# Optimization experiments

Hardware: AMD Instinct MI355X
Metric: run time of the kernel (lower is better)

The kernel has to match this reference:

```python
import jax, jax.numpy as jnp
import numpy as np

N = 50000      # nodes
E = 400000     # edges per edge type
T = 4          # edge types: add/sub/mul/div
F_IN = 128     # in_channels
H = 2          # heads
C = 64         # hidden_channels (per head)
HC = H * C     # 128
MLP = C // 8   # hidden_channels // 8 = 8
NUM_CLASSES = 10


def _glorot(key, shape):
    fan_in, fan_out = shape[-2], shape[-1]
    s = jnp.sqrt(6.0 / (fan_in + fan_out))
    return jax.random.uniform(key, shape, jnp.float32, -s, s)


def setup_inputs() -> dict:
    key = jax.random.key(0)
    ks = jax.random.split(key, 12)
    x = jax.random.normal(ks[0], (N, F_IN), jnp.float32)
    edge_index = jax.random.randint(ks[1], (T, 2, E), 0, N, jnp.int32)
    # layer-1 GATv2 params, stacked over the 4 edge types
    Wl1 = _glorot(ks[2], (T, F_IN, HC))
    Wr1 = _glorot(ks[3], (T, F_IN, HC))
    att1 = _glorot(ks[4], (T, H, C))
    b1 = jnp.zeros((T, HC), jnp.float32)
    # layer-2 GATv2 params (input dim = hidden*heads)
    Wl2 = _glorot(ks[5], (T, HC, HC))
    Wr2 = _glorot(ks[6], (T, HC, HC))
    att2 = _glorot(ks[7], (T, H, C))
    b2 = jnp.zeros((T, HC), jnp.float32)
    # MLP head
    W_lin1 = _glorot(ks[8], (HC, MLP))
    b_lin1 = jnp.zeros((MLP,), jnp.float32)
    W_lin2 = _glorot(ks[9], (MLP, NUM_CLASSES))
    b_lin2 = jnp.zeros((NUM_CLASSES,), jnp.float32)
    return dict(x=x, edge_index=edge_index, Wl1=Wl1, Wr1=Wr1, att1=att1, b1=b1,
                Wl2=Wl2, Wr2=Wr2, att2=att2, b2=b2,
                W_lin1=W_lin1, b_lin1=b_lin1, W_lin2=W_lin2, b_lin2=b_lin2)


def gatv2_conv(x, src, dst, Wl, Wr, att, bias):
    """PyG GATv2Conv: add self-loops, per-edge LeakyReLU attention,
    softmax over incoming edges per destination, weighted scatter-add."""
    n = x.shape[0]
    xl = (x @ Wl).reshape(n, H, C)   # source transform
    xr = (x @ Wr).reshape(n, H, C)   # destination transform
    loop = jnp.arange(n, dtype=src.dtype)
    s = jnp.concatenate([src, loop])
    d = jnp.concatenate([dst, loop])
    e = jax.nn.leaky_relu(xl[s] + xr[d], 0.2)          # [E+n, H, C]
    score = jnp.einsum('ehc,hc->eh', e, att)           # [E+n, H]
    smax = jax.ops.segment_max(score, d, num_segments=n)  # [N, H]
    p = jnp.exp(score - smax[d])                       # stable softmax numerators
    denom = jax.ops.segment_sum(p, d, num_segments=n)  # [N, H]
    msg = jax.ops.segment_sum(p[:, :, None] * xl[s], d, num_segments=n)  # [N, H, C]
    out = msg / denom[:, :, None]
    return out.reshape(n, HC) + bias


def hetero_layer(x, edge_index, Wl, Wr, att, b):
    # HeteroConv with aggr='sum' over the 4 edge types (single node type)
    out = gatv2_conv(x, edge_index[0, 0], edge_index[0, 1], Wl[0], Wr[0], att[0], b[0])
    for t in range(1, T):
        out = out + gatv2_conv(x, edge_index[t, 0], edge_index[t, 1], Wl[t], Wr[t], att[t], b[t])
    return out


def reference(x, edge_index, Wl1, Wr1, att1, b1, Wl2, Wr2, att2, b2,
              W_lin1, b_lin1, W_lin2, b_lin2):
    h = jax.nn.relu(hetero_layer(x, edge_index, Wl1, Wr1, att1, b1))
    h = jax.nn.relu(hetero_layer(h, edge_index, Wl2, Wr2, att2, b2))
    h = jax.nn.relu(h @ W_lin1 + b_lin1)
    # dropout p=0.5 is identity at eval time
    return h @ W_lin2 + b_lin2
```

## Files before the change

kernel.cpp:

```cpp
#include <hip/hip_runtime.h>
#include <hip/hip_bf16.h>
#include <math.h>

#define NN 50000
#define EE 400000
#define TT 4
#define FD 128
#define RPS 50004
#define NBKT 196
#define BCAP 4096
#define LOG2E 1.44269504f

typedef __attribute__((ext_vector_type(8))) short bf16x8;
typedef __attribute__((ext_vector_type(4))) float f32x4;

__device__ inline float bf2f(unsigned short u) {
  union { unsigned int i; float f; } x; x.i = ((unsigned int)u) << 16; return x.f;
}
__device__ inline unsigned short f2bf(float f) {
  __hip_bfloat16 h = __float2bfloat16(f);
  unsigned short u; __builtin_memcpy(&u, &h, 2); return u;
}
__device__ inline float blo(unsigned int u) {
  union { unsigned int i; float f; } x; x.i = u << 16; return x.f;
}
__device__ inline float bhi(unsigned int u) {
  union { unsigned int i; float f; } x; x.i = u & 0xFFFF0000u; return x.f;
}
__device__ inline float fexp2(float x) { return __builtin_amdgcn_exp2f(x); }
__device__ inline float sgn04(float a) {
  union { float f; unsigned int i; } x; x.f = a;
  x.i = (x.i & 0x80000000u) | 0x3ECCCCCDu;
  return x.f;
}
__device__ inline float qsum16(float v) {
  v += __builtin_bit_cast(float, __builtin_amdgcn_update_dpp(
         0, __builtin_bit_cast(int, v), 0xB1, 0xF, 0xF, true));
  v += __builtin_bit_cast(float, __builtin_amdgcn_update_dpp(
         0, __builtin_bit_cast(int, v), 0x4E, 0xF, 0xF, true));
  v += __builtin_bit_cast(float, __builtin_amdgcn_update_dpp(
         0, __builtin_bit_cast(int, v), 0x141, 0xF, 0xF, true));
  v += __builtin_bit_cast(float, __builtin_amdgcn_update_dpp(
         0, __builtin_bit_cast(int, v), 0x140, 0xF, 0xF, true));
  return v;
}

__global__ void k_cvtW(const float* __restrict__ Wl1, const float* __restrict__ Wr1,
                       const float* __restrict__ Wl2, const float* __restrict__ Wr2,
                       unsigned short* __restrict__ Bpack) {
  const int idx = blockIdx.x * 256 + threadIdx.x;
  const int R = idx >> 14;
  const int kc = idx & 16383;
  const int lr = R & 1, t = (R >> 1) & 3, layer = R >> 3;
  const float* W = layer ? (lr ? Wr2 : Wl2) : (lr ? Wr1 : Wl1);
  const float v = W[t * 16384 + kc];
  const int k = kc >> 7, c = kc & 127;
  const int nt = c >> 4, ks = k >> 5, g = (k >> 3) & 3, j = k & 7;
  const int lane = g * 16 + (c & 15);
  Bpack[(size_t)R * 16384 + ((nt * 4 + ks) * 64 + lane) * 8 + j] = f2bf(v);
}

__global__ void k_cvtA(const float* __restrict__ src, unsigned short* __restrict__ ahi,
                       unsigned short* __restrict__ alo) {
  const int idx = blockIdx.x * 256 + threadIdx.x;
  float4 v = ((const float4*)src)[idx];
  const unsigned short h0 = f2bf(v.x), h1 = f2bf(v.y), h2 = f2bf(v.z), h3 = f2bf(v.w);
  const unsigned short l0 = f2bf(v.x - bf2f(h0)), l1 = f2bf(v.y - bf2f(h1));
  const unsigned short l2 = f2bf(v.z - bf2f(h2)), l3 = f2bf(v.w - bf2f(h3));
  uint2 hv, lv;
  hv.x = (unsigned)h0 | ((unsigned)h1 << 16); hv.y = (unsigned)h2 | ((unsigned)h3 << 16);
  lv.x = (unsigned)l0 | ((unsigned)l1 << 16); lv.y = (unsigned)l2 | ((unsigned)l3 << 16);
  ((uint2*)ahi)[idx] = hv;
  ((uint2*)alo)[idx] = lv;
}

__global__ __launch_bounds__(128) void k_gemm4(
    const unsigned short* __restrict__ Ahi, const unsigned short* __restrict__ Alo,
    const unsigned short* __restrict__ Bbase,
    unsigned short* __restrict__ xl4, unsigned short* __restrict__ xr4) {
  const int t = blockIdx.y;
  const unsigned short* Bpt = Bbase + (size_t)t * 2 * 16384;
  unsigned short* xl = xl4 + (size_t)t * NN * FD;
  unsigned short* xr = xr4 + (size_t)t * NN * FD;
  const int tid = threadIdx.x;
  const int lane = tid & 63;
  const int w = tid >> 6;
  const int rh = lane & 15, g = lane >> 4;
  const int m0 = blockIdx.x * 64 + w * 32;
  f32x4 acc[2][16];
  #pragma unroll
  for (int a = 0; a < 2; ++a)
    #pragma unroll
    for (int b = 0; b < 16; ++b) acc[a][b] = (f32x4){0.f, 0.f, 0.f, 0.f};
  int r0 = m0 + rh;      if (r0 > NN - 1) r0 = NN - 1;
  int r1 = m0 + 16 + rh; if (r1 > NN - 1) r1 = NN - 1;
  #pragma unroll
  for (int ks = 0; ks < 4; ++ks) {
    const int ko = ks * 32 + g * 8;
    const bf16x8 ah0 = *(const bf16x8*)(Ahi + (size_t)r0 * FD + ko);
    const bf16x8 al0 = *(const bf16x8*)(Alo + (size_t)r0 * FD + ko);
    const bf16x8 ah1 = *(const bf16x8*)(Ahi + (size_t)r1 * FD + ko);
    const bf16x8 al1 = *(const bf16x8*)(Alo + (size_t)r1 * FD + ko);
    #pragma unroll
    for (int nt = 0; nt < 16; ++nt) {
      const bf16x8 b = *(const bf16x8*)(Bpt + (nt >> 3) * 16384 +
                                        (((nt & 7) * 4 + ks) * 64 + lane) * 8);
      acc[0][nt] = __builtin_amdgcn_mfma_f32_16x16x32_bf16(ah0, b, acc[0][nt], 0, 0, 0);
      acc[0][nt] = __builtin_amdgcn_mfma_f32_16x16x32_bf16(al0, b, acc[0][nt], 0, 0, 0);
      acc[1][nt] = __builtin_amdgcn_mfma_f32_16x16x32_bf16(ah1, b, acc[1][nt], 0, 0, 0);
      acc[1][nt] = __builtin_amdgcn_mfma_f32_16x16x32_bf16(al1, b, acc[1][nt], 0, 0, 0);
    }
  }
  #pragma unroll
  for (int mt = 0; mt < 2; ++mt)
    #pragma unroll
    for (int nt = 0; nt < 16; ++nt) {
      unsigned short* op = (nt < 8) ? xl : xr;
      const int cb = (nt & 7) * 16 + rh;
      #pragma unroll
      for (int r = 0; r < 4; ++r) {
        const int row = m0 + mt * 16 + g * 4 + r;
        if (row < NN) op[(size_t)row * FD + cb] = f2bf(acc[mt][nt][r]);
      }
    }
}

__global__ __launch_bounds__(256) void k_bucket(const int* __restrict__ ei,
                                                int* __restrict__ bcur,
                                                unsigned int* __restrict__ ebuf) {
  __shared__ int lcnt[NBKT], lbase[NBKT];
  const int t = blockIdx.y, tid = threadIdx.x;
  const int cbase = blockIdx.x * 4096;
  if (tid < NBKT) lcnt[tid] = 0;
  __syncthreads();
  const int* srcp = ei + (size_t)t * 2 * EE;
  const int* dstp = srcp + EE;
  unsigned int pk[16]; int rk[16];
  #pragma unroll
  for (int i = 0; i < 16; ++i) {
    const int e = cbase + i * 256 + tid;
    rk[i] = -1;
    if (e < EE) {
      const int s = srcp[e], dd = dstp[e];
      const int b = dd >> 8;
      pk[i] = ((unsigned)dd << 16) | (unsigned)s;
      rk[i] = (atomicAdd(&lcnt[b], 1) << 8) | b;
    }
  }
  __syncthreads();
  if (tid < NBKT && lcnt[tid] > 0) lbase[tid] = atomicAdd(&bcur[t * NBKT + tid], lcnt[tid]);
  __syncthreads();
  #pragma unroll
  for (int i = 0; i < 16; ++i) {
    if (rk[i] >= 0) {
      const int b = rk[i] & 255, r = rk[i] >> 8;
      ebuf[((size_t)t * NBKT + b) * BCAP + lbase[b] + r] = pk[i];
    }
  }
}

__global__ void k_bktscan(const int* __restrict__ bcur, int* __restrict__ bbase) {
  __shared__ int s[TT * NBKT];
  const int tid = threadIdx.x;
  int v0 = 0;
  if (tid < TT * NBKT) { v0 = bcur[tid]; s[tid] = v0; }
  __syncthreads();
  #pragma unroll
  for (int off = 1; off < NBKT; off <<= 1) {
    int a = 0;
    if (tid < TT * NBKT && (tid % NBKT) >= off) a = s[tid - off];
    __syncthreads();
    if (tid < TT * NBKT) s[tid] += a;
    __syncthreads();
  }
  if (tid < TT * NBKT) bbase[tid] = s[tid] - v0;
}

__global__ __launch_bounds__(256) void k_scatter3(const unsigned int* __restrict__ ebuf,
                                                  const int* __restrict__ bcur,
                                                  const int* __restrict__ bbase,
                                                  int* __restrict__ rowp,
                                                  int* __restrict__ col) {
  __shared__ int lc[256], sc[256];
  const int b = blockIdx.x, t = blockIdx.y, tid = threadIdx.x;
  const int d0 = b << 8;
  const int nd = (NN - d0 < 256) ? (NN - d0) : 256;
  const int cnt = bcur[t * NBKT + b];
  const int base = bbase[t * NBKT + b];
  const unsigned int* eb = ebuf + ((size_t)t * NBKT + b) * BCAP;
  lc[tid] = 0;
  __syncthreads();
  for (int j = tid; j < cnt; j += 256) {
    atomicAdd(&lc[(eb[j] >> 16) - d0], 1);
  }
  __syncthreads();
  const int v = lc[tid];
  sc[tid] = v;
  __syncthreads();
  #pragma unroll
  for (int off = 1; off < 256; off <<= 1) {
    const int a = (tid >= off) ? sc[tid - off] : 0;
    __syncthreads();
    sc[tid] += a;
    __syncthreads();
  }
  const int excl = base + sc[tid] - v;
  if (tid < nd) rowp[(size_t)t * RPS + d0 + tid] = excl;
  if (b == NBKT - 1 && tid == 0) rowp[(size_t)t * RPS + NN] = EE;
  lc[tid] = excl;
  __syncthreads();
  for (int j = tid; j < cnt; j += 256) {
    const unsigned int u = eb[j];
    const int pos = atomicAdd(&lc[(u >> 16) - d0], 1);
    col[(size_t)t * EE + pos] = (int)(u & 0xFFFF);
  }
}

__global__ __launch_bounds__(256) void k_agg5(
    const unsigned short* __restrict__ xl4, const unsigned short* __restrict__ xr4,
    const int* __restrict__ col, const int* __restrict__ rowp,
    const float* __restrict__ att, const float* __restrict__ bias,
    unsigned short* __restrict__ ahi, unsigned short* __restrict__ alo,
    float* __restrict__ hout, const int mode) {
  const int lane = threadIdx.x & 63;
  const int d = blockIdx.x * 4 + (threadIdx.x >> 6);
  const int head = (lane >> 4) & 1, sub = lane & 15, pbit = lane >> 5;
  const int laneoff = head * 128 + sub * 8;
  const int choff = head * 64 + sub * 4;
  float o0 = 0.f, o1 = 0.f, o2 = 0.f, o3 = 0.f;
  for (int t = 0; t < TT; ++t) {
    const char* xlt = (const char*)xl4 + ((size_t)t * NN) * 256 + laneoff;
    const char* xrt = (const char*)xr4 + ((size_t)t * NN) * 256 + laneoff;
    const int* colt = col + (size_t)t * EE;
    float4 av = *(const float4*)(att + t * FD + choff);
    av.x *= LOG2E; av.y *= LOG2E; av.z *= LOG2E; av.w *= LOG2E;
    const float sa0 = sgn04(av.x), sa1 = sgn04(av.y);
    const float sa2 = sgn04(av.z), sa3 = sgn04(av.w);
    const uint2 ur = *(const uint2*)(xrt + (size_t)d * 256);
    const float axr0 = av.x * blo(ur.x), axr1 = av.y * bhi(ur.x);
    const float axr2 = av.z * blo(ur.y), axr3 = av.w * bhi(ur.y);
    const uint2 us = *(const uint2*)(xlt + (size_t)d * 256);
    const float xs0 = blo(us.x), xs1 = bhi(us.x), xs2 = blo(us.y), xs3 = bhi(us.y);
    {
      const float q0 = fmaf(av.x, xs0, axr0), q1 = fmaf(av.y, xs1, axr1);
      const float q2 = fmaf(av.z, xs2, axr2), q3 = fmaf(av.w, xs3, axr3);
      float r = sa0 * fabsf(q0);
      r = fmaf(sa1, fabsf(q1), r); r = fmaf(sa2, fabsf(q2), r); r = fmaf(sa3, fabsf(q3), r);
      const float c = qsum16(fmaf(0.6f, (q0 + q1) + (q2 + q3), r));
      const bool isA = (pbit == 0);
      float m = isA ? c : -3.0e38f;
      float den = isA ? 1.f : 0.f;
      float a0 = isA ? xs0 : 0.f, a1 = isA ? xs1 : 0.f;
      float a2 = isA ? xs2 : 0.f, a3 = isA ? xs3 : 0.f;
      const int beg = rowp[(size_t)t * RPS + d];
      const int end = rowp[(size_t)t * RPS + d + 1];
      for (int eb = beg; eb < end; eb += 2) {
        const int e = eb + pbit;
        const bool act = (e < end);
        const int ec = act ? e : end - 1;
        const int s = colt[ec];
        const uint2 u = *(const uint2*)(xlt + (size_t)s * 256);
        const float x0 = blo(u.x), x1 = bhi(u.x), x2 = blo(u.y), x3 = bhi(u.y);
        const float q0 = fmaf(av.x, x0, axr0), q1 = fmaf(av.y, x1, axr1);
        const float q2 = fmaf(av.z, x2, axr2), q3 = fmaf(av.w, x3, axr3);
        float r = sa0 * fabsf(q0);
        r = fmaf(sa1, fabsf(q1), r); r = fmaf(sa2, fabsf(q2), r); r = fmaf(sa3, fabsf(q3), r);
        float c2 = qsum16(fmaf(0.6f, (q0 + q1) + (q2 + q3), r));
        const float p = act ? c2 : -INFINITY;
        const float nm = fmaxf(m, p);
        const float scl = fexp2(m - nm), w = fexp2(p - nm);
        den = fmaf(den, scl, w);
        a0 = fmaf(a0, scl, w * x0); a1 = fmaf(a1, scl, w * x1);
        a2 = fmaf(a2, scl, w * x2); a3 = fmaf(a3, scl, w * x3);
        m = nm;
      }
      const float mo = __shfl_xor(m, 32), deno = __shfl_xor(den, 32);
      const float b0 = __shfl_xor(a0, 32), b1 = __shfl_xor(a1, 32);
      const float b2 = __shfl_xor(a2, 32), b3 = __shfl_xor(a3, 32);
      const float nm = fmaxf(m, mo);
      const float sMe = fexp2(m - nm), sOt = fexp2(mo - nm);
      const float dm = fmaf(den, sMe, deno * sOt);
      const float rden = __builtin_amdgcn_rcpf(dm);
      o0 = fmaf(fmaf(a0, sMe, b0 * sOt), rden, o0);
      o1 = fmaf(fmaf(a1, sMe, b1 * sOt), rden, o1);
      o2 = fmaf(fmaf(a2, sMe, b2 * sOt), rden, o2);
      o3 = fmaf(fmaf(a3, sMe, b3 * sOt), rden, o3);
    }
  }
  #pragma unroll
  for (int t = 0; t < TT; ++t) {
    const float4 bv = *(const float4*)(bias + t * FD + choff);
    o0 += bv.x; o1 += bv.y; o2 += bv.z; o3 += bv.w;
  }
  if (pbit == 0) {
    if (mode == 0) {
      o0 = fmaxf(o0, 0.f); o1 = fmaxf(o1, 0.f);
      o2 = fmaxf(o2, 0.f); o3 = fmaxf(o3, 0.f);
      const unsigned short h0 = f2bf(o0), h1 = f2bf(o1);
      const unsigned short h2 = f2bf(o2), h3 = f2bf(o3);
      const unsigned short l0 = f2bf(o0 - bf2f(h0)), l1 = f2bf(o1 - bf2f(h1));
      const unsigned short l2 = f2bf(o2 - bf2f(h2)), l3 = f2bf(o3 - bf2f(h3));
      uint2 hv, lv;
      hv.x = (unsigned)h0 | ((unsigned)h1 << 16); hv.y = (unsigned)h2 | ((unsigned)h3 << 16);
      lv.x = (unsigned)l0 | ((unsigned)l1 << 16); lv.y = (unsigned)l2 | ((unsigned)l3 << 16);
      const size_t ui = (size_t)d * 64 + head * 32 + sub * 2;
      ((uint2*)((unsigned int*)ahi + ui))[0] = hv;
      ((uint2*)((unsigned int*)alo + ui))[0] = lv;
    } else {
      *(float4*)(hout + (size_t)d * FD + choff) = make_float4(o0, o1, o2, o3);
    }
  }
}

__global__ __launch_bounds__(256) void k_mlp(const float* __restrict__ h,
                                             const float* __restrict__ W1,
                                             const float* __restrict__ b1,
                                             const float* __restrict__ W2,
                                             const float* __restrict__ b2,
                                             float* __restrict__ out) {
  __shared__ float sW1[128 * 8];
  __shared__ float sW2[8 * 10];
  __shared__ float sb1[8], sb2[10];
  for (int i = threadIdx.x; i < 1024; i += 256) sW1[i] = W1[i];
  if (threadIdx.x < 80) sW2[threadIdx.x] = W2[threadIdx.x];
  if (threadIdx.x < 8)  sb1[threadIdx.x] = b1[threadIdx.x];
  if (threadIdx.x < 10) sb2[threadIdx.x] = b2[threadIdx.x];
  __syncthreads();
  const int n = blockIdx.x * 256 + threadIdx.x;
  if (n >= NN) return;
  const float* hn = h + (size_t)n * FD;
  float z[8];
  #pragma unroll
  for (int j = 0; j < 8; ++j) z[j] = sb1[j];
  for (int k = 0; k < FD; k += 4) {
    float4 hv = *(const float4*)(hn + k);
    hv.x = fmaxf(hv.x, 0.f); hv.y = fmaxf(hv.y, 0.f);
    hv.z = fmaxf(hv.z, 0.f); hv.w = fmaxf(hv.w, 0.f);
    #pragma unroll
    for (int j = 0; j < 8; ++j) {
      z[j] += hv.x * sW1[(k + 0) * 8 + j] + hv.y * sW1[(k + 1) * 8 + j]
            + hv.z * sW1[(k + 2) * 8 + j] + hv.w * sW1[(k + 3) * 8 + j];
    }
  }
  #pragma unroll
  for (int j = 0; j < 8; ++j) z[j] = fmaxf(z[j], 0.f);
  float o[10];
  #pragma unroll
  for (int c = 0; c < 10; ++c) o[c] = sb2[c];
  #pragma unroll
  for (int j = 0; j < 8; ++j)
    #pragma unroll
    for (int c = 0; c < 10; ++c) o[c] += z[j] * sW2[j * 10 + c];
  float* op = out + (size_t)n * 10;
  #pragma unroll
  for (int c = 0; c < 10; ++c) op[c] = o[c];
}

extern "C" void kernel_launch(void* const* d_in, const int* in_sizes, int n_in,
                              void* d_out, int out_size, void* d_ws, size_t ws_size,
                              hipStream_t stream) {
  const float* x    = (const float*)d_in[0];
  const int*   ei   = (const int*)d_in[1];
  const float* Wl1  = (const float*)d_in[2];
  const float* Wr1  = (const float*)d_in[3];
  const float* att1 = (const float*)d_in[4];
  const float* b1   = (const float*)d_in[5];
  const float* Wl2  = (const float*)d_in[6];
  const float* Wr2  = (const float*)d_in[7];
  const float* att2 = (const float*)d_in[8];
  const float* b2   = (const float*)d_in[9];
  const float* Wi1  = (const float*)d_in[10];
  const float* bi1  = (const float*)d_in[11];
  const float* Wi2  = (const float*)d_in[12];
  const float* bi2  = (const float*)d_in[13];
  float* out = (float*)d_out;

  char* ws = (char*)d_ws;
  size_t off = 0;
  auto alloc = [&](size_t bytes) {
    void* p = ws + off;
    off = (off + bytes + 255) & ~(size_t)255;
    return p;
  };
  unsigned short* xl4   = (unsigned short*)alloc((size_t)TT * NN * FD * 2);
  unsigned short* xr4   = (unsigned short*)alloc((size_t)TT * NN * FD * 2);
  unsigned short* Ahi   = (unsigned short*)alloc((size_t)NN * FD * 2);
  unsigned short* Alo   = (unsigned short*)alloc((size_t)NN * FD * 2);
  unsigned short* Bpack = (unsigned short*)alloc((size_t)2 * TT * 2 * 16384 * 2);
  int*            col   = (int*)alloc((size_t)TT * EE * 4);
  int*            rowp  = (int*)alloc((size_t)TT * RPS * 4);
  int*            bcur  = (int*)alloc((size_t)TT * NBKT * 4);
  int*            bbase = (int*)alloc((size_t)TT * NBKT * 4);
  unsigned int*   ebuf  = (unsigned int*)alloc((size_t)TT * NBKT * BCAP * 4);
  float* h2 = (float*)Ahi;

  hipMemsetAsync(bcur, 0, (size_t)TT * NBKT * 4, stream);
  k_cvtW<<<1024, 256, 0, stream>>>(Wl1, Wr1, Wl2, Wr2, Bpack);
  k_bucket<<<dim3(98, TT), 256, 0, stream>>>(ei, bcur, ebuf);
  k_bktscan<<<1, 1024, 0, stream>>>(bcur, bbase);
  k_scatter3<<<dim3(NBKT, TT), 256, 0, stream>>>(ebuf, bcur, bbase, rowp, col);

  k_cvtA<<<6250, 256, 0, stream>>>(x, Ahi, Alo);
  k_gemm4<<<dim3(782, TT), 128, 0, stream>>>(Ahi, Alo, Bpack, xl4, xr4);
  k_agg5<<<12500, 256, 0, stream>>>(xl4, xr4, col, rowp, att1, b1,
                                    Ahi, Alo, nullptr, 0);
  k_gemm4<<<dim3(782, TT), 128, 0, stream>>>(Ahi, Alo, Bpack + (size_t)TT * 2 * 16384,
                                             xl4, xr4);
  k_agg5<<<12500, 256, 0, stream>>>(xl4, xr4, col, rowp, att2, b2,
                                    nullptr, nullptr, h2, 1);
  k_mlp<<<(NN + 255) / 256, 256, 0, stream>>>(h2, Wi1, bi1, Wi2, bi2, out);
}
```

Measured before the change: 570.6 us.

## Fold self-loops into CSR and aggregate four edges per wave without running max

```diff
diff --git a/kernel.cpp b/kernel.cpp
--- a/kernel.cpp
+++ b/kernel.cpp
@@ -4,6 +4,7 @@
 
 #define NN 50000
 #define EE 400000
+#define EEN 450000
 #define TT 4
 #define FD 128
 #define RPS 50004
@@ -33,16 +34,18 @@
   x.i = (x.i & 0x80000000u) | 0x3ECCCCCDu;
   return x.f;
 }
-__device__ inline float qsum16(float v) {
+__device__ inline float qsum8(float v) {
   v += __builtin_bit_cast(float, __builtin_amdgcn_update_dpp(
          0, __builtin_bit_cast(int, v), 0xB1, 0xF, 0xF, true));
   v += __builtin_bit_cast(float, __builtin_amdgcn_update_dpp(
          0, __builtin_bit_cast(int, v), 0x4E, 0xF, 0xF, true));
   v += __builtin_bit_cast(float, __builtin_amdgcn_update_dpp(
          0, __builtin_bit_cast(int, v), 0x141, 0xF, 0xF, true));
-  v += __builtin_bit_cast(float, __builtin_amdgcn_update_dpp(
-         0, __builtin_bit_cast(int, v), 0x140, 0xF, 0xF, true));
   return v;
+}
+__device__ inline void unpack8(const uint4 u, float* x) {
+  x[0] = blo(u.x); x[1] = bhi(u.x); x[2] = blo(u.y); x[3] = bhi(u.y);
+  x[4] = blo(u.z); x[5] = bhi(u.z); x[6] = blo(u.w); x[7] = bhi(u.w);
 }
 
 __global__ void k_cvtW(const float* __restrict__ Wl1, const float* __restrict__ Wr1,
@@ -140,8 +143,10 @@
   for (int i = 0; i < 16; ++i) {
     const int e = cbase + i * 256 + tid;
     rk[i] = -1;
-    if (e < EE) {
-      const int s = srcp[e], dd = dstp[e];
+    if (e < EEN) {
+      int s, dd;
+      if (e < EE) { s = srcp[e]; dd = dstp[e]; }
+      else        { s = dd = e - EE; }
       const int b = dd >> 8;
       pk[i] = ((unsigned)dd << 16) | (unsigned)s;
       rk[i] = (atomicAdd(&lcnt[b], 1) << 8) | b;
@@ -206,17 +211,17 @@
   }
   const int excl = base + sc[tid] - v;
   if (tid < nd) rowp[(size_t)t * RPS + d0 + tid] = excl;
-  if (b == NBKT - 1 && tid == 0) rowp[(size_t)t * RPS + NN] = EE;
+  if (b == NBKT - 1 && tid == 0) rowp[(size_t)t * RPS + NN] = EEN;
   lc[tid] = excl;
   __syncthreads();
   for (int j = tid; j < cnt; j += 256) {
     const unsigned int u = eb[j];
     const int pos = atomicAdd(&lc[(u >> 16) - d0], 1);
-    col[(size_t)t * EE + pos] = (int)(u & 0xFFFF);
-  }
-}
-
-__global__ __launch_bounds__(256) void k_agg5(
+    col[(size_t)t * EEN + pos] = (int)(u & 0xFFFF);
+  }
+}
+
+__global__ __launch_bounds__(256) void k_agg6(
     const unsigned short* __restrict__ xl4, const unsigned short* __restrict__ xr4,
     const int* __restrict__ col, const int* __restrict__ rowp,
     const float* __restrict__ att, const float* __restrict__ bias,
@@ -224,90 +229,93 @@
     float* __restrict__ hout, const int mode) {
   const int lane = threadIdx.x & 63;
   const int d = blockIdx.x * 4 + (threadIdx.x >> 6);
-  const int head = (lane >> 4) & 1, sub = lane & 15, pbit = lane >> 5;
-  const int laneoff = head * 128 + sub * 8;
-  const int choff = head * 64 + sub * 4;
-  float o0 = 0.f, o1 = 0.f, o2 = 0.f, o3 = 0.f;
+  const int g = lane >> 3;
+  const int slot = g >> 1, head = g & 1, sub = lane & 7;
+  const int laneoff = head * 128 + sub * 16;
+  const int choff = head * 64 + sub * 8;
+  float o[8];
+  #pragma unroll
+  for (int j = 0; j < 8; ++j) o[j] = 0.f;
+  #pragma unroll
   for (int t = 0; t < TT; ++t) {
-    const char* xlt = (const char*)xl4 + ((size_t)t * NN) * 256 + laneoff;
-    const char* xrt = (const char*)xr4 + ((size_t)t * NN) * 256 + laneoff;
-    const int* colt = col + (size_t)t * EE;
-    float4 av = *(const float4*)(att + t * FD + choff);
-    av.x *= LOG2E; av.y *= LOG2E; av.z *= LOG2E; av.w *= LOG2E;
-    const float sa0 = sgn04(av.x), sa1 = sgn04(av.y);
-    const float sa2 = sgn04(av.z), sa3 = sgn04(av.w);
-    const uint2 ur = *(const uint2*)(xrt + (size_t)d * 256);
-    const float axr0 = av.x * blo(ur.x), axr1 = av.y * bhi(ur.x);
-    const float axr2 = av.z * blo(ur.y), axr3 = av.w * bhi(ur.y);
-    const uint2 us = *(const uint2*)(xlt + (size_t)d * 256);
-    const float xs0 = blo(us.x), xs1 = bhi(us.x), xs2 = blo(us.y), xs3 = bhi(us.y);
-    {
-      const float q0 = fmaf(av.x, xs0, axr0), q1 = fmaf(av.y, xs1, axr1);
-      const float q2 = fmaf(av.z, xs2, axr2), q3 = fmaf(av.w, xs3, axr3);
-      float r = sa0 * fabsf(q0);
-      r = fmaf(sa1, fabsf(q1), r); r = fmaf(sa2, fabsf(q2), r); r = fmaf(sa3, fabsf(q3), r);
-      const float c = qsum16(fmaf(0.6f, (q0 + q1) + (q2 + q3), r));
-      const bool isA = (pbit == 0);
-      float m = isA ? c : -3.0e38f;
-      float den = isA ? 1.f : 0.f;
-      float a0 = isA ? xs0 : 0.f, a1 = isA ? xs1 : 0.f;
-      float a2 = isA ? xs2 : 0.f, a3 = isA ? xs3 : 0.f;
-      const int beg = rowp[(size_t)t * RPS + d];
-      const int end = rowp[(size_t)t * RPS + d + 1];
-      for (int eb = beg; eb < end; eb += 2) {
-        const int e = eb + pbit;
-        const bool act = (e < end);
-        const int ec = act ? e : end - 1;
-        const int s = colt[ec];
-        const uint2 u = *(const uint2*)(xlt + (size_t)s * 256);
-        const float x0 = blo(u.x), x1 = bhi(u.x), x2 = blo(u.y), x3 = bhi(u.y);
-        const float q0 = fmaf(av.x, x0, axr0), q1 = fmaf(av.y, x1, axr1);
-        const float q2 = fmaf(av.z, x2, axr2), q3 = fmaf(av.w, x3, axr3);
-        float r = sa0 * fabsf(q0);
-        r = fmaf(sa1, fabsf(q1), r); r = fmaf(sa2, fabsf(q2), r); r = fmaf(sa3, fabsf(q3), r);
-        float c2 = qsum16(fmaf(0.6f, (q0 + q1) + (q2 + q3), r));
-        const float p = act ? c2 : -INFINITY;
-        const float nm = fmaxf(m, p);
-        const float scl = fexp2(m - nm), w = fexp2(p - nm);
-        den = fmaf(den, scl, w);
-        a0 = fmaf(a0, scl, w * x0); a1 = fmaf(a1, scl, w * x1);
-        a2 = fmaf(a2, scl, w * x2); a3 = fmaf(a3, scl, w * x3);
-        m = nm;
+    const char* xlt = (const char*)xl4 + (size_t)t * NN * 256 + laneoff;
+    const char* xrt = (const char*)xr4 + (size_t)t * NN * 256 + laneoff;
+    const int* colt = col + (size_t)t * EEN;
+    const float4 a0 = *(const float4*)(att + t * FD + choff);
+    const float4 a1 = *(const float4*)(att + t * FD + choff + 4);
+    float av[8] = {a0.x, a0.y, a0.z, a0.w, a1.x, a1.y, a1.z, a1.w};
+    const uint4 ur = *(const uint4*)(xrt + (size_t)d * 256);
+    float xrv[8]; unpack8(ur, xrv);
+    float sa[8], axr[8];
+    #pragma unroll
+    for (int j = 0; j < 8; ++j) {
+      av[j] *= LOG2E; sa[j] = sgn04(av[j]); axr[j] = av[j] * xrv[j];
+    }
+    float den = 0.f, acc[8];
+    #pragma unroll
+    for (int j = 0; j < 8; ++j) acc[j] = 0.f;
+    const int beg = rowp[t * RPS + d];
+    const int end = rowp[t * RPS + d + 1];
+    for (int e0 = beg; e0 < end; e0 += 4) {
+      const int e = e0 + slot;
+      const bool act = e < end;
+      const int s = colt[act ? e : end - 1];
+      const uint4 u = *(const uint4*)(xlt + ((size_t)((unsigned)s << 8)));
+      float x[8]; unpack8(u, x);
+      float s06 = 0.f, sr = 0.f;
+      #pragma unroll
+      for (int j = 0; j < 8; ++j) {
+        const float q = fmaf(av[j], x[j], axr[j]);
+        s06 += q;
+        sr = fmaf(sa[j], fabsf(q), sr);
       }
-      const float mo = __shfl_xor(m, 32), deno = __shfl_xor(den, 32);
-      const float b0 = __shfl_xor(a0, 32), b1 = __shfl_xor(a1, 32);
-      const float b2 = __shfl_xor(a2, 32), b3 = __shfl_xor(a3, 32);
-      const float nm = fmaxf(m, mo);
-      const float sMe = fexp2(m - nm), sOt = fexp2(mo - nm);
-      const float dm = fmaf(den, sMe, deno * sOt);
-      const float rden = __builtin_amdgcn_rcpf(dm);
-      o0 = fmaf(fmaf(a0, sMe, b0 * sOt), rden, o0);
-      o1 = fmaf(fmaf(a1, sMe, b1 * sOt), rden, o1);
-      o2 = fmaf(fmaf(a2, sMe, b2 * sOt), rden, o2);
-      o3 = fmaf(fmaf(a3, sMe, b3 * sOt), rden, o3);
-    }
+      const float c = qsum8(fmaf(0.6f, s06, sr));
+      const float w = act ? fexp2(c) : 0.f;
+      den += w;
+      #pragma unroll
+      for (int j = 0; j < 8; ++j) acc[j] = fmaf(w, x[j], acc[j]);
+    }
+    den += __shfl_xor(den, 16);
+    den += __shfl_xor(den, 32);
+    const float rden = __builtin_amdgcn_rcpf(den);
+    #pragma unroll
+    for (int j = 0; j < 8; ++j) o[j] = fmaf(acc[j], rden, o[j]);
+  }
+  #pragma unroll
+  for (int j = 0; j < 8; ++j) {
+    o[j] += __shfl_xor(o[j], 16);
+    o[j] += __shfl_xor(o[j], 32);
   }
   #pragma unroll
   for (int t = 0; t < TT; ++t) {
-    const float4 bv = *(const float4*)(bias + t * FD + choff);
-    o0 += bv.x; o1 += bv.y; o2 += bv.z; o3 += bv.w;
-  }
-  if (pbit == 0) {
+    const float4 b0 = *(const float4*)(bias + t * FD + choff);
+    const float4 b1 = *(const float4*)(bias + t * FD + choff + 4);
+    o[0] += b0.x; o[1] += b0.y; o[2] += b0.z; o[3] += b0.w;
+    o[4] += b1.x; o[5] += b1.y; o[6] += b1.z; o[7] += b1.w;
+  }
+  if (lane < 16) {
     if (mode == 0) {
-      o0 = fmaxf(o0, 0.f); o1 = fmaxf(o1, 0.f);
-      o2 = fmaxf(o2, 0.f); o3 = fmaxf(o3, 0.f);
-      const unsigned short h0 = f2bf(o0), h1 = f2bf(o1);
-      const unsigned short h2 = f2bf(o2), h3 = f2bf(o3);
-      const unsigned short l0 = f2bf(o0 - bf2f(h0)), l1 = f2bf(o1 - bf2f(h1));
-      const unsigned short l2 = f2bf(o2 - bf2f(h2)), l3 = f2bf(o3 - bf2f(h3));
-      uint2 hv, lv;
-      hv.x = (unsigned)h0 | ((unsigned)h1 << 16); hv.y = (unsigned)h2 | ((unsigned)h3 << 16);
-      lv.x = (unsigned)l0 | ((unsigned)l1 << 16); lv.y = (unsigned)l2 | ((unsigned)l3 << 16);
-      const size_t ui = (size_t)d * 64 + head * 32 + sub * 2;
-      ((uint2*)((unsigned int*)ahi + ui))[0] = hv;
-      ((uint2*)((unsigned int*)alo + ui))[0] = lv;
+      unsigned short hs[8], ls[8];
+      #pragma unroll
+      for (int j = 0; j < 8; ++j) {
+        const float r = fmaxf(o[j], 0.f);
+        hs[j] = f2bf(r);
+        ls[j] = f2bf(r - bf2f(hs[j]));
+      }
+      uint4 hv, lv;
+      hv.x = (unsigned)hs[0] | ((unsigned)hs[1] << 16);
+      hv.y = (unsigned)hs[2] | ((unsigned)hs[3] << 16);
+      hv.z = (unsigned)hs[4] | ((unsigned)hs[5] << 16);
+      hv.w = (unsigned)hs[6] | ((unsigned)hs[7] << 16);
+      lv.x = (unsigned)ls[0] | ((unsigned)ls[1] << 16);
+      lv.y = (unsigned)ls[2] | ((unsigned)ls[3] << 16);
+      lv.z = (unsigned)ls[4] | ((unsigned)ls[5] << 16);
+      lv.w = (unsigned)ls[6] | ((unsigned)ls[7] << 16);
+      *(uint4*)((char*)ahi + (size_t)d * 256 + laneoff) = hv;
+      *(uint4*)((char*)alo + (size_t)d * 256 + laneoff) = lv;
     } else {
-      *(float4*)(hout + (size_t)d * FD + choff) = make_float4(o0, o1, o2, o3);
+      *(float4*)(hout + (size_t)d * FD + choff) = make_float4(o[0], o[1], o[2], o[3]);
+      *(float4*)(hout + (size_t)d * FD + choff + 4) = make_float4(o[4], o[5], o[6], o[7]);
     }
   }
 }
@@ -387,7 +395,7 @@
   unsigned short* Ahi   = (unsigned short*)alloc((size_t)NN * FD * 2);
   unsigned short* Alo   = (unsigned short*)alloc((size_t)NN * FD * 2);
   unsigned short* Bpack = (unsigned short*)alloc((size_t)2 * TT * 2 * 16384 * 2);
-  int*            col   = (int*)alloc((size_t)TT * EE * 4);
+  int*            col   = (int*)alloc((size_t)TT * EEN * 4);
   int*            rowp  = (int*)alloc((size_t)TT * RPS * 4);
   int*            bcur  = (int*)alloc((size_t)TT * NBKT * 4);
   int*            bbase = (int*)alloc((size_t)TT * NBKT * 4);
@@ -396,17 +404,17 @@
 
   hipMemsetAsync(bcur, 0, (size_t)TT * NBKT * 4, stream);
   k_cvtW<<<1024, 256, 0, stream>>>(Wl1, Wr1, Wl2, Wr2, Bpack);
-  k_bucket<<<dim3(98, TT), 256, 0, stream>>>(ei, bcur, ebuf);
+  k_bucket<<<dim3(110, TT), 256, 0, stream>>>(ei, bcur, ebuf);
   k_bktscan<<<1, 1024, 0, stream>>>(bcur, bbase);
   k_scatter3<<<dim3(NBKT, TT), 256, 0, stream>>>(ebuf, bcur, bbase, rowp, col);
 
   k_cvtA<<<6250, 256, 0, stream>>>(x, Ahi, Alo);
   k_gemm4<<<dim3(782, TT), 128, 0, stream>>>(Ahi, Alo, Bpack, xl4, xr4);
-  k_agg5<<<12500, 256, 0, stream>>>(xl4, xr4, col, rowp, att1, b1,
+  k_agg6<<<12500, 256, 0, stream>>>(xl4, xr4, col, rowp, att1, b1,
                                     Ahi, Alo, nullptr, 0);
   k_gemm4<<<dim3(782, TT), 128, 0, stream>>>(Ahi, Alo, Bpack + (size_t)TT * 2 * 16384,
                                              xl4, xr4);
-  k_agg5<<<12500, 256, 0, stream>>>(xl4, xr4, col, rowp, att2, b2,
+  k_agg6<<<12500, 256, 0, stream>>>(xl4, xr4, col, rowp, att2, b2,
                                     nullptr, nullptr, h2, 1);
   k_mlp<<<(NN + 255) / 256, 256, 0, stream>>>(h2, Wi1, bi1, Wi2, bi2, out);
 }
```

New measurement: 646.8 us. +13.3%, slower.
